# Kernel tuning notes

Hardware: AMD Instinct MI355X
Metric: run time of the kernel (lower is better)

Reference implementation:

```python
import jax, jax.numpy as jnp
import numpy as np

B, T_ENC, C, H, NSTEPS, NCLS, NEMB = 512, 64, 512, 512, 26, 97, 256


def setup_inputs() -> dict:
    key = jax.random.key(0)
    ks = jax.random.split(key, 20)
    w = lambda k, shape, s=0.05: jax.random.normal(k, shape, dtype=jnp.float32) * s
    return {
        "batch_H": jax.random.normal(ks[0], (B, T_ENC, C), dtype=jnp.float32),
        "Attentive_Sequence": jax.random.normal(ks[1], (B, NSTEPS, H), dtype=jnp.float32),
        "text": jax.random.randint(ks[2], (B, NSTEPS), 0, NCLS),
        "W_i2h": w(ks[3], (H, C)),                      # i2h, bias=False
        "W_h2h": w(ks[4], (H, H)), "b_h2h": w(ks[5], (H,)),
        "w_score": w(ks[6], (H,)),                      # score Linear(H,1), bias=False
        "W_ih": w(ks[7], (4 * H, C + NEMB)), "W_hh": w(ks[8], (4 * H, H)),
        "b_ih": w(ks[9], (4 * H,)), "b_hh": w(ks[10], (4 * H,)),
        "Wf1": w(ks[11], (H, H)), "bf1": w(ks[12], (H,)),   # GatedBimodal branch 1
        "Wf2": w(ks[13], (H, H)), "bf2": w(ks[14], (H,)),   # GatedBimodal branch 2
        "Wz": w(ks[15], (H, 2 * H)), "bz": w(ks[16], (H,)),  # gate over concat
        "W_gen": w(ks[17], (NCLS, H)), "b_gen": w(ks[18], (NCLS,)),
        "emb_table": w(ks[19], (NCLS + 1, NEMB), 1.0),
    }


def reference(batch_H, Attentive_Sequence, text, W_i2h, W_h2h, b_h2h, w_score,
              W_ih, W_hh, b_ih, b_hh, Wf1, bf1, Wf2, bf2, Wz, bz,
              W_gen, b_gen, emb_table):
    b = batch_H.shape[0]
    char_embs = emb_table[text]                                  # [B, NSTEPS, NEMB]
    H_proj = jnp.einsum('btc,hc->bth', batch_H, W_i2h)           # i2h once (loop-invariant)
    h0 = jnp.zeros((b, H), jnp.float32)
    c0 = jnp.zeros((b, H), jnp.float32)

    def step(carry, xs):
        h, c = carry
        emb_t, seq_t = xs                                        # [B,NEMB], [B,H]
        hp = h @ W_h2h.T + b_h2h                                 # h2h
        e = jnp.tanh(H_proj + hp[:, None, :]) @ w_score          # [B, T_ENC]
        alpha = jax.nn.softmax(e, axis=1)
        context = jnp.einsum('bt,btc->bc', alpha, batch_H)       # bmm(alpha^T, H)
        # GatedBimodal fusion
        f1 = jnp.tanh(context @ Wf1.T + bf1)
        f2 = jnp.tanh(seq_t @ Wf2.T + bf2)
        z = jax.nn.sigmoid(jnp.concatenate([context, seq_t], axis=1) @ Wz.T + bz)
        I_char = z * f1 + (1.0 - z) * f2
        # LSTMCell
        x = jnp.concatenate([I_char, emb_t], axis=1)
        gates = x @ W_ih.T + b_ih + h @ W_hh.T + b_hh
        i_g, f_g, g_g, o_g = jnp.split(gates, 4, axis=1)
        c_new = jax.nn.sigmoid(f_g) * c + jax.nn.sigmoid(i_g) * jnp.tanh(g_g)
        h_new = jax.nn.sigmoid(o_g) * jnp.tanh(c_new)
        return (h_new, c_new), (h_new, alpha, I_char)

    xs = (jnp.swapaxes(char_embs, 0, 1), jnp.swapaxes(Attentive_Sequence, 0, 1))
    _, (hs, alphas, chars) = jax.lax.scan(step, (h0, c0), xs)
    output_hiddens = jnp.swapaxes(hs, 0, 1)                      # [B, NSTEPS, H]
    seq_attention_map = jnp.transpose(alphas, (1, 2, 0))         # [B, T_ENC, NSTEPS]
    Char = jnp.swapaxes(chars, 0, 1)                             # [B, NSTEPS, H]
    probs = output_hiddens @ W_gen.T + b_gen                     # [B, NSTEPS, NCLS]
    return probs, seq_attention_map, output_hiddens, Char
```

## Files before the change

### kernel.cpp

```cpp
#include <hip/hip_runtime.h>

#define NS_ 26
#define NCLS_ 97

typedef short bf16x8 __attribute__((ext_vector_type(8)));
typedef float f32x4 __attribute__((ext_vector_type(4)));

__device__ __forceinline__ unsigned short f2bf(float f) {
  union { float f; unsigned u; } v; v.f = f;
  unsigned r = v.u + 0x7fffu + ((v.u >> 16) & 1u);
  return (unsigned short)(r >> 16);
}
__device__ __forceinline__ float bf2f(unsigned short h) {
  union { unsigned u; float f; } v; v.u = ((unsigned)h) << 16;
  return v.f;
}
__device__ __forceinline__ float sigm_f(float x) { return 1.f / (1.f + __expf(-x)); }
__device__ __forceinline__ float tanh_f(float x) { return 1.f - 2.f / (1.f + __expf(2.f * x)); }

__device__ __forceinline__ void gl_lds16(const void* g, void* l) {
  __builtin_amdgcn_global_load_lds(
      (const __attribute__((address_space(1))) unsigned int*)g,
      (__attribute__((address_space(3))) unsigned int*)l, 16, 0, 0);
}

template <bool OUTF>
__global__ __launch_bounds__(256) void gemm_tiled_k(
    const unsigned short* __restrict__ Ag, const unsigned short* __restrict__ Bg,
    const float* __restrict__ bias, float* __restrict__ outF,
    unsigned short* __restrict__ outB, int K, long ldo, int Nvalid) {
  __shared__ unsigned short As[128 * 64];
  __shared__ unsigned short Bs[128 * 64];
  const int tid = threadIdx.x;
  const int w = tid >> 6, l = tid & 63;
  const int l15 = l & 15, lq = l >> 4;
  const int wm = w >> 1, wn = w & 1;
  const long rowBase = (long)blockIdx.y * 128;
  const long colBase = (long)blockIdx.x * 128;
  const int lrow = l >> 3, ps_st = l & 7;
  f32x4 acc[4][4] = {};
  for (int kt = 0; kt < K; kt += 64) {
#pragma unroll
    for (int i = 0; i < 4; ++i) {
      const int row = i * 32 + w * 8 + lrow;
      const int ls = ps_st ^ (row & 7);
      gl_lds16(Ag + (rowBase + row) * K + kt + ls * 8, As + i * 2048 + w * 512);
      gl_lds16(Bg + (colBase + row) * K + kt + ls * 8, Bs + i * 2048 + w * 512);
    }
    __syncthreads();
#pragma unroll
    for (int kh = 0; kh < 2; ++kh) {
      bf16x8 af[4], bfr[4];
#pragma unroll
      for (int mi = 0; mi < 4; ++mi) {
        const int row = wm * 64 + mi * 16 + l15;
        const int ps = (kh * 4 + lq) ^ (row & 7);
        af[mi] = *(const bf16x8*)(As + row * 64 + ps * 8);
      }
#pragma unroll
      for (int ni = 0; ni < 4; ++ni) {
        const int row = wn * 64 + ni * 16 + l15;
        const int ps = (kh * 4 + lq) ^ (row & 7);
        bfr[ni] = *(const bf16x8*)(Bs + row * 64 + ps * 8);
      }
#pragma unroll
      for (int mi = 0; mi < 4; ++mi)
#pragma unroll
        for (int ni = 0; ni < 4; ++ni)
          acc[mi][ni] = __builtin_amdgcn_mfma_f32_16x16x32_bf16(af[mi], bfr[ni], acc[mi][ni], 0, 0, 0);
    }
    __syncthreads();
  }
#pragma unroll
  for (int mi = 0; mi < 4; ++mi)
#pragma unroll
    for (int ni = 0; ni < 4; ++ni) {
      const long gcol = colBase + wn * 64 + ni * 16 + l15;
      if (gcol >= Nvalid) continue;
      const float bv = bias ? bias[gcol] : 0.f;
#pragma unroll
      for (int r = 0; r < 4; ++r) {
        const long grow = rowBase + wm * 64 + mi * 16 + lq * 4 + r;
        const float v = acc[mi][ni][r] + bv;
        if (OUTF) outF[grow * ldo + gcol] = v;
        else      outB[grow * ldo + gcol] = f2bf(v);
      }
    }
}

__global__ __launch_bounds__(1024, 4) void attn_fused_k(
    const unsigned short* __restrict__ hrd, const unsigned short* __restrict__ Wt4,
    const float* __restrict__ b_h2h, const unsigned short* __restrict__ Hproj,
    const unsigned short* __restrict__ bH, const float* __restrict__ w_score,
    float* __restrict__ attn_map, unsigned short* __restrict__ ctx, int s) {
  const long b0 = (long)blockIdx.x * 2;
  const int tid = threadIdx.x;
  __shared__ float hs[1024];
  __shared__ float hp_t[1040];
  __shared__ float ws_t[520];
  __shared__ float e_s[128];
  __shared__ float csum[1024];
  hs[tid] = bf2f(hrd[b0 * 512 + tid]);
  if (tid < 512) ws_t[(tid & 7) * 65 + (tid >> 3)] = w_score[tid];
  __syncthreads();
  {
    const int pair = tid >> 9, j = tid & 511;
    float acc = b_h2h[j];
    const unsigned short* wp = Wt4 + j * 4;
    const float* hv0 = hs + pair * 512;
#pragma unroll 8
    for (int k4 = 0; k4 < 128; ++k4) {
      const ushort4 wv = *(const ushort4*)(wp + k4 * 2048);
      const f32x4 hv = *(const f32x4*)(hv0 + k4 * 4);
      acc += bf2f(wv.x) * hv[0] + bf2f(wv.y) * hv[1]
           + bf2f(wv.z) * hv[2] + bf2f(wv.w) * hv[3];
    }
    hp_t[pair * 520 + (j & 7) * 65 + (j >> 3)] = acc;
  }
  __syncthreads();
  const int w16 = tid >> 6, l = tid & 63;
  const int srow = w16 >> 3;
  const float* hpT = hp_t + srow * 520;
#pragma unroll
  for (int tt = 0; tt < 8; ++tt) {
    const int t = (w16 & 7) * 8 + tt;
    const bf16x8 hv = *(const bf16x8*)(Hproj + ((b0 + srow) * 64 + t) * 512 + l * 8);
    float acc = 0.f;
#pragma unroll
    for (int j = 0; j < 8; ++j)
      acc += tanh_f(bf2f((unsigned short)hv[j]) + hpT[j * 65 + l]) * ws_t[j * 65 + l];
    acc += __shfl_xor(acc, 1);
    acc += __shfl_xor(acc, 2);
    acc += __shfl_xor(acc, 4);
    acc += __shfl_xor(acc, 8);
    acc += __shfl_xor(acc, 16);
    acc += __shfl_xor(acc, 32);
    if (l == 0) e_s[srow * 64 + t] = acc;
  }
  __syncthreads();
  if ((w16 & 7) == 0) {
    const int row = w16 >> 3;
    const float e = e_s[row * 64 + l];
    float m = e;
    for (int off = 32; off; off >>= 1) m = fmaxf(m, __shfl_xor(m, off));
    const float p = __expf(e - m);
    float sum = p;
    for (int off = 32; off; off >>= 1) sum += __shfl_xor(sum, off);
    const float a = p / sum;
    e_s[row * 64 + l] = a;
    attn_map[((b0 + row) * 64 + l) * NS_ + s] = a;
  }
  __syncthreads();
  {
    const int row = tid >> 9, st = tid & 511;
    const int half = st >> 8, jj = st & 255;
    float c0 = 0.f, c1 = 0.f;
    const unsigned* bhp = (const unsigned*)(bH + ((b0 + row) * 64 + half * 32) * 512) + jj;
    const float* al = e_s + row * 64 + half * 32;
#pragma unroll 8
    for (int t = 0; t < 32; ++t) {
      const float a = al[t];
      const unsigned pv = bhp[(long)t * 256];
      c0 += a * bf2f((unsigned short)(pv & 0xffffu));
      c1 += a * bf2f((unsigned short)(pv >> 16));
    }
    if (half) { csum[row * 512 + jj * 2] = c0; csum[row * 512 + jj * 2 + 1] = c1; }
    __syncthreads();
    if (!half) {
      c0 += csum[row * 512 + jj * 2];
      c1 += csum[row * 512 + jj * 2 + 1];
      ((unsigned*)ctx)[(b0 + row) * 256 + jj] = (unsigned)f2bf(c0) | ((unsigned)f2bf(c1) << 16);
    }
  }
}

__global__ __launch_bounds__(512, 4) void gated_fused_k(
    const unsigned short* __restrict__ ctx, const unsigned short* __restrict__ Wfz,
    const unsigned short* __restrict__ FZpre, const float* __restrict__ bf1,
    unsigned short* __restrict__ Ichar, float* __restrict__ Char_out, int s) {
  __shared__ float ls[2 * 16 * 65];
  const int tid = threadIdx.x, w = tid >> 6, l = tid & 63, l15 = l & 15, lq = l >> 4;
  const int b0 = blockIdx.y * 16, j0 = blockIdx.x * 64;
  const int which = w >> 2, nh = w & 3;
  f32x4 acc = {};
  const long arow = b0 + l15;
  const long gw = (long)(which ? 512 : 0) + j0 + nh * 16 + l15;
#pragma unroll
  for (int kt = 0; kt < 512; kt += 64) {
    const int k0 = kt + lq * 8, k1 = k0 + 32;
    const bf16x8 a0 = *(const bf16x8*)(ctx + arow * 512 + k0);
    const bf16x8 a1 = *(const bf16x8*)(ctx + arow * 512 + k1);
    const bf16x8 w0 = *(const bf16x8*)(Wfz + gw * 512 + k0);
    const bf16x8 w1 = *(const bf16x8*)(Wfz + gw * 512 + k1);
    acc = __builtin_amdgcn_mfma_f32_16x16x32_bf16(a0, w0, acc, 0, 0, 0);
    acc = __builtin_amdgcn_mfma_f32_16x16x32_bf16(a1, w1, acc, 0, 0, 0);
  }
#pragma unroll
  for (int r = 0; r < 4; ++r)
    ls[which * 1040 + (lq * 4 + r) * 65 + nh * 16 + l15] = acc[r];
  __syncthreads();
#pragma unroll
  for (int i = 0; i < 2; ++i) {
    const int e = tid + i * 512;
    const int r = e >> 6, c = e & 63;
    const long b = b0 + r;
    const int j = j0 + c;
    const float f1 = tanh_f(ls[r * 65 + c] + bf1[j]);
    const float zc = ls[1040 + r * 65 + c];
    const long pr = (b * NS_ + s) * 1024;
    const float f2 = tanh_f(bf2f(FZpre[pr + j]));
    const float z = sigm_f(zc + bf2f(FZpre[pr + 512 + j]));
    const float I = z * f1 + (1.f - z) * f2;
    Char_out[(b * NS_ + s) * 512 + j] = I;
    Ichar[b * 512 + j] = f2bf(I);
  }
}

__global__ __launch_bounds__(512, 4) void gates_lstm_k(
    const unsigned short* __restrict__ Ichar, const unsigned short* __restrict__ embb,
    const unsigned short* __restrict__ hrd, const unsigned short* __restrict__ Wihh,
    const float* __restrict__ biasG, float* __restrict__ cbuf,
    float* __restrict__ hid_out, unsigned short* __restrict__ hwr, int s) {
  __shared__ float gs[4 * 32 * 33];
  const int tid = threadIdx.x, w = tid >> 6, l = tid & 63, l15 = l & 15, lq = l >> 4;
  const int b0 = blockIdx.y * 32, j0 = blockIdx.x * 32;
  const int g = w & 3, mi = w >> 2;
  const long arow = b0 + mi * 16 + l15;
  const unsigned short* iptr = Ichar + arow * 512;
  const unsigned short* eptr = embb + (arow * NS_ + s) * 256 - 512;
  const unsigned short* hptr = hrd + arow * 512 - 768;
  const unsigned short* wptr = Wihh + ((long)g * 512 + j0 + l15) * 1280;
  f32x4 acc[2] = {};
#pragma unroll
  for (int kt = 0; kt < 1280; kt += 64) {
    const int k0 = kt + lq * 8, k1 = k0 + 32;
    bf16x8 a0, a1, b0r[2], b1r[2];
    a0 = (k0 < 512) ? *(const bf16x8*)(iptr + k0)
       : (k0 < 768) ? *(const bf16x8*)(eptr + k0)
                    : *(const bf16x8*)(hptr + k0);
    a1 = (k1 < 512) ? *(const bf16x8*)(iptr + k1)
       : (k1 < 768) ? *(const bf16x8*)(eptr + k1)
                    : *(const bf16x8*)(hptr + k1);
#pragma unroll
    for (int ni = 0; ni < 2; ++ni) {
      b0r[ni] = *(const bf16x8*)(wptr + (long)ni * 16 * 1280 + k0);
      b1r[ni] = *(const bf16x8*)(wptr + (long)ni * 16 * 1280 + k1);
    }
#pragma unroll
    for (int ni = 0; ni < 2; ++ni) {
      acc[ni] = __builtin_amdgcn_mfma_f32_16x16x32_bf16(a0, b0r[ni], acc[ni], 0, 0, 0);
      acc[ni] = __builtin_amdgcn_mfma_f32_16x16x32_bf16(a1, b1r[ni], acc[ni], 0, 0, 0);
    }
  }
#pragma unroll
  for (int ni = 0; ni < 2; ++ni)
#pragma unroll
    for (int r = 0; r < 4; ++r) {
      const int rl = mi * 16 + lq * 4 + r;
      const int cl = ni * 16 + l15;
      gs[(g * 32 + rl) * 33 + cl] = acc[ni][r];
    }
  __syncthreads();
#pragma unroll
  for (int i = 0; i < 2; ++i) {
    const int e = tid + i * 512;
    const int r = e >> 5, c = e & 31;
    const long b = b0 + r;
    const int j = j0 + c;
    const float ig = sigm_f(gs[(0 * 32 + r) * 33 + c] + biasG[j]);
    const float fg = sigm_f(gs[(1 * 32 + r) * 33 + c] + biasG[512 + j]);
    const float gg = tanh_f(gs[(2 * 32 + r) * 33 + c] + biasG[1024 + j]);
    const float og = sigm_f(gs[(3 * 32 + r) * 33 + c] + biasG[1536 + j]);
    const float cn = fg * cbuf[b * 512 + j] + ig * gg;
    cbuf[b * 512 + j] = cn;
    const float h = og * tanh_f(cn);
    hid_out[(b * NS_ + s) * 512 + j] = h;
    hwr[b * 512 + j] = f2bf(h);
  }
}

__global__ __launch_bounds__(256) void probs_k(
    const float* __restrict__ Af, const unsigned short* __restrict__ Wg,
    const float* __restrict__ bias, float* __restrict__ outp) {
  const int tid = threadIdx.x, w = tid >> 6, l = tid & 63, l15 = l & 15, lq = l >> 4;
  const long mrow = (long)blockIdx.y * 64 + w * 16 + l15;
  const int nbase = blockIdx.x * 64;
  f32x4 acc[4] = {};
  for (int kt = 0; kt < 512; kt += 32) {
    const int k = kt + lq * 8;
    const float4 av0 = *(const float4*)(Af + mrow * 512 + k);
    const float4 av1 = *(const float4*)(Af + mrow * 512 + k + 4);
    bf16x8 a;
    a[0] = (short)f2bf(av0.x); a[1] = (short)f2bf(av0.y);
    a[2] = (short)f2bf(av0.z); a[3] = (short)f2bf(av0.w);
    a[4] = (short)f2bf(av1.x); a[5] = (short)f2bf(av1.y);
    a[6] = (short)f2bf(av1.z); a[7] = (short)f2bf(av1.w);
#pragma unroll
    for (int nb = 0; nb < 4; ++nb) {
      const bf16x8 b = *(const bf16x8*)(Wg + (long)(nbase + nb * 16 + l15) * 512 + k);
      acc[nb] = __builtin_amdgcn_mfma_f32_16x16x32_bf16(a, b, acc[nb], 0, 0, 0);
    }
  }
#pragma unroll
  for (int nb = 0; nb < 4; ++nb) {
    const int colg = nbase + nb * 16 + l15;
    if (colg >= NCLS_) continue;
    const float bv = bias[colg];
#pragma unroll
    for (int r = 0; r < 4; ++r) {
      const long rowg = (long)blockIdx.y * 64 + w * 16 + lq * 4 + r;
      outp[rowg * NCLS_ + colg] = acc[nb][r] + bv;
    }
  }
}

#define CVT_N0 4194304L
#define CVT_N1 1703936L
#define CVT_N2 65536L
__global__ void mega_cvt_k(const float* __restrict__ batch_H, const float* __restrict__ AS,
                           const float* __restrict__ W_i2h,
                           unsigned short* __restrict__ bH, unsigned short* __restrict__ ASb,
                           unsigned short* __restrict__ Wi2hb) {
  const long q = (long)blockIdx.x * 256 + threadIdx.x;
  const float* src; unsigned short* dst; long i;
  if (q < CVT_N0) { src = batch_H; dst = bH; i = q; }
  else if (q < CVT_N0 + CVT_N1) { src = AS; dst = ASb; i = q - CVT_N0; }
  else if (q < CVT_N0 + CVT_N1 + CVT_N2) { src = W_i2h; dst = Wi2hb; i = q - CVT_N0 - CVT_N1; }
  else return;
  const float4 v = *(const float4*)(src + i * 4);
  ushort4 o;
  o.x = f2bf(v.x); o.y = f2bf(v.y); o.z = f2bf(v.z); o.w = f2bf(v.w);
  *(ushort4*)(dst + i * 4) = o;
}

#define PK_N0 2621440L
#define PK_N1 524288L
#define PK_N2 524288L
#define PK_N3 65536L
#define PK_N4 262144L
#define PK_N5 3072L
#define PK_N6 3407872L
__global__ void mega_pack_k(
    const float* __restrict__ W_ih, const float* __restrict__ W_hh,
    const float* __restrict__ Wf1, const float* __restrict__ Wf2,
    const float* __restrict__ Wz, const float* __restrict__ W_gen,
    const float* __restrict__ W_h2h,
    const float* __restrict__ b_ih, const float* __restrict__ b_hh,
    const float* __restrict__ bf2, const float* __restrict__ bz,
    const float* __restrict__ emb_table, const int* __restrict__ text,
    unsigned short* __restrict__ Wihh, unsigned short* __restrict__ Wfz,
    unsigned short* __restrict__ Wfz2, unsigned short* __restrict__ Wgenb,
    unsigned short* __restrict__ Wt4, float* __restrict__ biasG,
    float* __restrict__ biasFZ, unsigned short* __restrict__ embb) {
  long q = (long)blockIdx.x * 256 + threadIdx.x;
  if (q < PK_N0) {
    const int row = (int)(q / 1280), c = (int)(q % 1280);
    const float v = (c < 768) ? W_ih[(long)row * 768 + c] : W_hh[(long)row * 512 + (c - 768)];
    Wihh[q] = f2bf(v);
    return;
  }
  q -= PK_N0;
  if (q < PK_N1) {
    const int row = (int)(q >> 9), k = (int)(q & 511);
    const float v = (row < 512) ? Wf1[(long)row * 512 + k] : Wz[(long)(row - 512) * 1024 + k];
    Wfz[q] = f2bf(v);
    return;
  }
  q -= PK_N1;
  if (q < PK_N2) {
    const int row = (int)(q >> 9), k = (int)(q & 511);
    const float v = (row < 512) ? Wf2[(long)row * 512 + k]
                                : Wz[(long)(row - 512) * 1024 + 512 + k];
    Wfz2[q] = f2bf(v);
    return;
  }
  q -= PK_N2;
  if (q < PK_N3) {
    const int row = (int)(q >> 9), k = (int)(q & 511);
    Wgenb[q] = (row < NCLS_) ? f2bf(W_gen[(long)row * 512 + k]) : (unsigned short)0;
    return;
  }
  q -= PK_N3;
  if (q < PK_N4) {
    const int j = (int)(q >> 9), k = (int)(q & 511);
    Wt4[((long)(k >> 2) * 2048) + j * 4 + (k & 3)] = f2bf(W_h2h[q]);
    return;
  }
  q -= PK_N4;
  if (q < PK_N5) {
    if (q < 2048) biasG[q] = b_ih[q] + b_hh[q];
    else {
      const int j = (int)(q - 2048);
      biasFZ[j] = (j < 512) ? bf2[j] : bz[j - 512];
    }
    return;
  }
  q -= PK_N5;
  if (q < PK_N6) {
    const long bs = q >> 8;
    const int j = (int)(q & 255);
    const int t = text[bs];
    embb[q] = f2bf(emb_table[(long)t * 256 + j]);
  }
}

extern "C" void kernel_launch(void* const* d_in, const int* in_sizes, int n_in,
                              void* d_out, int out_size, void* d_ws, size_t ws_size,
                              hipStream_t stream) {
  (void)in_sizes; (void)n_in; (void)out_size; (void)ws_size;
  const float* batch_H  = (const float*)d_in[0];
  const float* AS       = (const float*)d_in[1];
  const int*   text     = (const int*)d_in[2];
  const float* W_i2h    = (const float*)d_in[3];
  const float* W_h2h    = (const float*)d_in[4];
  const float* b_h2h    = (const float*)d_in[5];
  const float* w_score  = (const float*)d_in[6];
  const float* W_ih     = (const float*)d_in[7];
  const float* W_hh     = (const float*)d_in[8];
  const float* b_ih     = (const float*)d_in[9];
  const float* b_hh     = (const float*)d_in[10];
  const float* Wf1      = (const float*)d_in[11];
  const float* bf1      = (const float*)d_in[12];
  const float* Wf2      = (const float*)d_in[13];
  const float* bf2      = (const float*)d_in[14];
  const float* Wz       = (const float*)d_in[15];
  const float* bz       = (const float*)d_in[16];
  const float* W_gen    = (const float*)d_in[17];
  const float* b_gen    = (const float*)d_in[18];
  const float* emb_tab  = (const float*)d_in[19];

  float* out = (float*)d_out;
  float* out_probs = out;
  float* out_attn  = out + 1291264;
  float* out_hid   = out + 2143232;
  float* out_char  = out + 8958976;

  char* wsp = (char*)d_ws;
  auto alloc = [&](size_t bytes) { char* p = wsp; wsp += (bytes + 255) & ~(size_t)255; return p; };
  unsigned short* bH    = (unsigned short*)alloc(33554432);
  unsigned short* Hproj = (unsigned short*)alloc(33554432);
  unsigned short* ASb   = (unsigned short*)alloc(13631488);
  unsigned short* embb  = (unsigned short*)alloc(6815744);
  unsigned short* FZpre = (unsigned short*)alloc(27262976);
  unsigned short* Wt4   = (unsigned short*)alloc(524288);
  unsigned short* Wfz   = (unsigned short*)alloc(1048576);
  unsigned short* Wfz2  = (unsigned short*)alloc(1048576);
  unsigned short* Wihh  = (unsigned short*)alloc(5242880);
  unsigned short* Wgenb = (unsigned short*)alloc(131072);
  unsigned short* Wi2hb = (unsigned short*)alloc(524288);
  float* biasG          = (float*)alloc(8192);
  float* biasFZ         = (float*)alloc(4096);
  char* ab = (char*)ASb;
  unsigned short* ctx   = (unsigned short*)(ab);
  unsigned short* Ichar = (unsigned short*)(ab + 524288);
  float* cbuf           = (float*)(ab + 1048576);
  unsigned short* hbuf  = (unsigned short*)(ab + 2097152);

  mega_cvt_k<<<dim3(23297), dim3(256), 0, stream>>>(batch_H, AS, W_i2h, bH, ASb, Wi2hb);
  mega_pack_k<<<dim3(28960), dim3(256), 0, stream>>>(
      W_ih, W_hh, Wf1, Wf2, Wz, W_gen, W_h2h, b_ih, b_hh, bf2, bz, emb_tab, text,
      Wihh, Wfz, Wfz2, Wgenb, Wt4, biasG, biasFZ, embb);

  gemm_tiled_k<false><<<dim3(4, 256), dim3(256), 0, stream>>>(
      bH, Wi2hb, nullptr, nullptr, Hproj, 512, 512, 512);

  gemm_tiled_k<false><<<dim3(8, 104), dim3(256), 0, stream>>>(
      ASb, Wfz2, biasFZ, nullptr, FZpre, 512, 1024, 1024);

  hipMemsetAsync(cbuf, 0, 1048576, stream);
  hipMemsetAsync(hbuf, 0, 1048576, stream);

  for (int s = 0; s < NS_; ++s) {
    unsigned short* hrd = hbuf + (s & 1) * 262144;
    unsigned short* hwr = hbuf + ((s + 1) & 1) * 262144;
    attn_fused_k<<<dim3(256), dim3(1024), 0, stream>>>(
        hrd, Wt4, b_h2h, Hproj, bH, w_score, out_attn, ctx, s);
    gated_fused_k<<<dim3(8, 32), dim3(512), 0, stream>>>(
        ctx, Wfz, FZpre, bf1, Ichar, out_char, s);
    gates_lstm_k<<<dim3(16, 16), dim3(512), 0, stream>>>(
        Ichar, embb, hrd, Wihh, biasG, cbuf, out_hid, hwr, s);
  }

  probs_k<<<dim3(2, 208), dim3(256), 0, stream>>>(out_hid, Wgenb, b_gen, out_probs);
}
```

Before: 2.010 ms.

## Fuse per-step recurrent kernels into one persistent cooperative kernel with group barriers

Replaces the 78 per-step kernel launches (attention, gated fusion, LSTM gates) with a single cooperative kernel that loops over all 26 steps. The batch is split into 8 independent groups of 32 blocks, each synchronised by a hand-written atomic barrier, and shared intermediates go through global memory with cache-bypassing loads and stores. The h2h projection becomes a separate MFMA phase that writes hp to global memory. This removes launch overhead and inter-kernel gaps, but adds four grid barriers per step, relies on all blocks being co-resident, and runs 1024-thread blocks with some threads idle in several phases.

```diff
diff --git a/kernel.cpp b/kernel.cpp
--- a/kernel.cpp
+++ b/kernel.cpp
@@ -22,6 +22,39 @@
   __builtin_amdgcn_global_load_lds(
       (const __attribute__((address_space(1))) unsigned int*)g,
       (__attribute__((address_space(3))) unsigned int*)l, 16, 0, 0);
+}
+
+__device__ __forceinline__ bf16x8 llcld(const unsigned short* p) {
+  bf16x8 v;
+  asm volatile("global_load_dwordx4 %0, %1, off sc0 sc1\ns_waitcnt vmcnt(0)"
+               : "=v"(v) : "v"(p) : "memory");
+  return v;
+}
+__device__ __forceinline__ void llcst(unsigned short* p, bf16x8 v) {
+  asm volatile("global_store_dwordx4 %0, %1, off sc0 sc1" :: "v"(p), "v"(v) : "memory");
+}
+__device__ __forceinline__ f32x4 llcldf(const float* p) {
+  f32x4 v;
+  asm volatile("global_load_dwordx4 %0, %1, off sc0 sc1\ns_waitcnt vmcnt(0)"
+               : "=v"(v) : "v"(p) : "memory");
+  return v;
+}
+__device__ __forceinline__ void llcstf(float* p, f32x4 v) {
+  asm volatile("global_store_dwordx4 %0, %1, off sc0 sc1" :: "v"(p), "v"(v) : "memory");
+}
+
+__device__ __forceinline__ void gbar(unsigned* bar, unsigned* gen, unsigned target) {
+  asm volatile("s_waitcnt vmcnt(0)" ::: "memory");
+  __syncthreads();
+  if (threadIdx.x == 0) {
+    const unsigned prev = __hip_atomic_fetch_add(bar, 1u, __ATOMIC_RELAXED, __HIP_MEMORY_SCOPE_AGENT);
+    if (prev + 1u == target * 32u) {
+      __hip_atomic_store(gen, target, __ATOMIC_RELAXED, __HIP_MEMORY_SCOPE_AGENT);
+    } else {
+      while (__hip_atomic_load(gen, __ATOMIC_RELAXED, __HIP_MEMORY_SCOPE_AGENT) < target) {}
+    }
+  }
+  __syncthreads();
 }
 
 template <bool OUTF>
@@ -88,194 +121,302 @@
     }
 }
 
-__global__ __launch_bounds__(1024, 4) void attn_fused_k(
-    const unsigned short* __restrict__ hrd, const unsigned short* __restrict__ Wt4,
-    const float* __restrict__ b_h2h, const unsigned short* __restrict__ Hproj,
-    const unsigned short* __restrict__ bH, const float* __restrict__ w_score,
-    float* __restrict__ attn_map, unsigned short* __restrict__ ctx, int s) {
-  const long b0 = (long)blockIdx.x * 2;
+struct CoopArgs {
+  const unsigned short* Hproj;
+  const unsigned short* bH;
+  const unsigned short* Wh2hb;
+  const unsigned short* Wfz;
+  const unsigned short* FZpre;
+  const unsigned short* Wihh;
+  const unsigned short* embb;
+  const float* b_h2h;
+  const float* w_score;
+  const float* bf1;
+  const float* biasG;
+  float* hp;
+  float* out_attn;
+  float* out_char;
+  float* out_hid;
+  float* cbuf;
+  unsigned short* ctx;
+  unsigned short* Ichar;
+  unsigned short* hbuf;
+  unsigned* bars;
+};
+
+__global__ __launch_bounds__(1024, 4) void scan_coop_k(CoopArgs A) {
+  __shared__ float ws_t[520];
+  __shared__ __align__(16) char smraw[52224];
   const int tid = threadIdx.x;
-  __shared__ float hs[1024];
-  __shared__ float hp_t[1040];
-  __shared__ float ws_t[520];
-  __shared__ float e_s[128];
-  __shared__ float csum[1024];
-  hs[tid] = bf2f(hrd[b0 * 512 + tid]);
-  if (tid < 512) ws_t[(tid & 7) * 65 + (tid >> 3)] = w_score[tid];
+  const int bx = blockIdx.x;
+  const int g = bx & 7, lb = bx >> 3;
+  const long rb = (long)g * 64;
+  unsigned* bar = A.bars + g * 32;
+  unsigned* gen = bar + 1;
+  unsigned tgt = 0;
+
+  if (tid < 512) ws_t[(tid & 7) * 65 + (tid >> 3)] = A.w_score[tid];
   __syncthreads();
-  {
-    const int pair = tid >> 9, j = tid & 511;
-    float acc = b_h2h[j];
-    const unsigned short* wp = Wt4 + j * 4;
-    const float* hv0 = hs + pair * 512;
+
+  for (int s = 0; s < NS_; ++s) {
+    const unsigned short* hrd = A.hbuf + (s & 1) * 262144;
+    unsigned short* hwr = A.hbuf + ((s + 1) & 1) * 262144;
+
+    {
+      const int bt = lb >> 3, jt = lb & 7;
+      const long b0 = rb + bt * 16;
+      const int j0 = jt * 64;
+      unsigned short* h16 = (unsigned short*)smraw;
+      float* ls = (float*)(smraw + 16640);
+      float* hpo = (float*)(smraw + 24960);
+      {
+        const int row = tid >> 6, c = tid & 63;
+        const bf16x8 v = llcld(hrd + (b0 + row) * 512 + c * 8);
+        *(bf16x8*)(h16 + row * 520 + c * 8) = v;
+      }
+      __syncthreads();
+      if (tid < 512) {
+        const int w = tid >> 6, l = tid & 63, l15 = l & 15, lq = l >> 4;
+        const int kh = w >> 2, ni = w & 3;
+        const unsigned short* wrow = A.Wh2hb + (long)(j0 + ni * 16 + l15) * 512 + kh * 256;
+        const unsigned short* arow = h16 + l15 * 520 + kh * 256;
+        f32x4 acc = {};
+#pragma unroll
+        for (int kt = 0; kt < 256; kt += 64) {
+          const int k0 = kt + lq * 8, k1 = k0 + 32;
+          const bf16x8 a0 = *(const bf16x8*)(arow + k0);
+          const bf16x8 a1 = *(const bf16x8*)(arow + k1);
+          const bf16x8 w0 = *(const bf16x8*)(wrow + k0);
+          const bf16x8 w1 = *(const bf16x8*)(wrow + k1);
+          acc = __builtin_amdgcn_mfma_f32_16x16x32_bf16(a0, w0, acc, 0, 0, 0);
+          acc = __builtin_amdgcn_mfma_f32_16x16x32_bf16(a1, w1, acc, 0, 0, 0);
+        }
+#pragma unroll
+        for (int r = 0; r < 4; ++r)
+          ls[kh * 1040 + (lq * 4 + r) * 65 + ni * 16 + l15] = acc[r];
+      }
+      __syncthreads();
+      {
+        const int r = tid >> 6, c = tid & 63;
+        hpo[r * 64 + c] = ls[r * 65 + c] + ls[1040 + r * 65 + c] + A.b_h2h[j0 + c];
+      }
+      __syncthreads();
+      if (tid < 256) {
+        const int row = tid >> 4, c = tid & 15;
+        const f32x4 v = *(const f32x4*)(hpo + row * 64 + c * 4);
+        llcstf(A.hp + (b0 + row) * 512 + j0 + c * 4, v);
+      }
+    }
+    gbar(bar, gen, ++tgt);
+
+    {
+      const long b0 = rb + lb * 2;
+      float* hp_t = (float*)smraw;
+      float* e_s  = (float*)(smraw + 4160);
+      float* csum = (float*)(smraw + 4672);
+      unsigned* pck = (unsigned*)(smraw + 8768);
+      if (tid < 256) {
+        const int row = tid >> 7, q = tid & 127;
+        const f32x4 v = llcldf(A.hp + (b0 + row) * 512 + q * 4);
+#pragma unroll
+        for (int i = 0; i < 4; ++i) {
+          const int j = q * 4 + i;
+          hp_t[row * 520 + (j & 7) * 65 + (j >> 3)] = v[i];
+        }
+      }
+      __syncthreads();
+      const int w16 = tid >> 6, l = tid & 63;
+      const int srow = w16 >> 3;
+      const float* hpT = hp_t + srow * 520;
+#pragma unroll
+      for (int tt = 0; tt < 8; ++tt) {
+        const int t = (w16 & 7) * 8 + tt;
+        const bf16x8 hv = *(const bf16x8*)(A.Hproj + ((b0 + srow) * 64 + t) * 512 + l * 8);
+        float acc = 0.f;
+#pragma unroll
+        for (int j = 0; j < 8; ++j)
+          acc += tanh_f(bf2f((unsigned short)hv[j]) + hpT[j * 65 + l]) * ws_t[j * 65 + l];
+        acc += __shfl_xor(acc, 1);
+        acc += __shfl_xor(acc, 2);
+        acc += __shfl_xor(acc, 4);
+        acc += __shfl_xor(acc, 8);
+        acc += __shfl_xor(acc, 16);
+        acc += __shfl_xor(acc, 32);
+        if (l == 0) e_s[srow * 64 + t] = acc;
+      }
+      __syncthreads();
+      if ((w16 & 7) == 0) {
+        const float e = e_s[srow * 64 + l];
+        float m = e;
+        for (int off = 32; off; off >>= 1) m = fmaxf(m, __shfl_xor(m, off));
+        const float p = __expf(e - m);
+        float sum = p;
+        for (int off = 32; off; off >>= 1) sum += __shfl_xor(sum, off);
+        const float a = p / sum;
+        e_s[srow * 64 + l] = a;
+        A.out_attn[((b0 + srow) * 64 + l) * NS_ + s] = a;
+      }
+      __syncthreads();
+      {
+        const int row = tid >> 9, st = tid & 511;
+        const int half = st >> 8, jj = st & 255;
+        float c0 = 0.f, c1 = 0.f;
+        const unsigned* bhp = (const unsigned*)(A.bH + ((b0 + row) * 64 + half * 32) * 512) + jj;
+        const float* al = e_s + row * 64 + half * 32;
 #pragma unroll 8
-    for (int k4 = 0; k4 < 128; ++k4) {
-      const ushort4 wv = *(const ushort4*)(wp + k4 * 2048);
-      const f32x4 hv = *(const f32x4*)(hv0 + k4 * 4);
-      acc += bf2f(wv.x) * hv[0] + bf2f(wv.y) * hv[1]
-           + bf2f(wv.z) * hv[2] + bf2f(wv.w) * hv[3];
-    }
-    hp_t[pair * 520 + (j & 7) * 65 + (j >> 3)] = acc;
-  }
-  __syncthreads();
-  const int w16 = tid >> 6, l = tid & 63;
-  const int srow = w16 >> 3;
-  const float* hpT = hp_t + srow * 520;
-#pragma unroll
-  for (int tt = 0; tt < 8; ++tt) {
-    const int t = (w16 & 7) * 8 + tt;
-    const bf16x8 hv = *(const bf16x8*)(Hproj + ((b0 + srow) * 64 + t) * 512 + l * 8);
-    float acc = 0.f;
-#pragma unroll
-    for (int j = 0; j < 8; ++j)
-      acc += tanh_f(bf2f((unsigned short)hv[j]) + hpT[j * 65 + l]) * ws_t[j * 65 + l];
-    acc += __shfl_xor(acc, 1);
-    acc += __shfl_xor(acc, 2);
-    acc += __shfl_xor(acc, 4);
-    acc += __shfl_xor(acc, 8);
-    acc += __shfl_xor(acc, 16);
-    acc += __shfl_xor(acc, 32);
-    if (l == 0) e_s[srow * 64 + t] = acc;
-  }
-  __syncthreads();
-  if ((w16 & 7) == 0) {
-    const int row = w16 >> 3;
-    const float e = e_s[row * 64 + l];
-    float m = e;
-    for (int off = 32; off; off >>= 1) m = fmaxf(m, __shfl_xor(m, off));
-    const float p = __expf(e - m);
-    float sum = p;
-    for (int off = 32; off; off >>= 1) sum += __shfl_xor(sum, off);
-    const float a = p / sum;
-    e_s[row * 64 + l] = a;
-    attn_map[((b0 + row) * 64 + l) * NS_ + s] = a;
-  }
-  __syncthreads();
-  {
-    const int row = tid >> 9, st = tid & 511;
-    const int half = st >> 8, jj = st & 255;
-    float c0 = 0.f, c1 = 0.f;
-    const unsigned* bhp = (const unsigned*)(bH + ((b0 + row) * 64 + half * 32) * 512) + jj;
-    const float* al = e_s + row * 64 + half * 32;
-#pragma unroll 8
-    for (int t = 0; t < 32; ++t) {
-      const float a = al[t];
-      const unsigned pv = bhp[(long)t * 256];
-      c0 += a * bf2f((unsigned short)(pv & 0xffffu));
-      c1 += a * bf2f((unsigned short)(pv >> 16));
-    }
-    if (half) { csum[row * 512 + jj * 2] = c0; csum[row * 512 + jj * 2 + 1] = c1; }
-    __syncthreads();
-    if (!half) {
-      c0 += csum[row * 512 + jj * 2];
-      c1 += csum[row * 512 + jj * 2 + 1];
-      ((unsigned*)ctx)[(b0 + row) * 256 + jj] = (unsigned)f2bf(c0) | ((unsigned)f2bf(c1) << 16);
-    }
-  }
-}
-
-__global__ __launch_bounds__(512, 4) void gated_fused_k(
-    const unsigned short* __restrict__ ctx, const unsigned short* __restrict__ Wfz,
-    const unsigned short* __restrict__ FZpre, const float* __restrict__ bf1,
-    unsigned short* __restrict__ Ichar, float* __restrict__ Char_out, int s) {
-  __shared__ float ls[2 * 16 * 65];
-  const int tid = threadIdx.x, w = tid >> 6, l = tid & 63, l15 = l & 15, lq = l >> 4;
-  const int b0 = blockIdx.y * 16, j0 = blockIdx.x * 64;
-  const int which = w >> 2, nh = w & 3;
-  f32x4 acc = {};
-  const long arow = b0 + l15;
-  const long gw = (long)(which ? 512 : 0) + j0 + nh * 16 + l15;
-#pragma unroll
-  for (int kt = 0; kt < 512; kt += 64) {
-    const int k0 = kt + lq * 8, k1 = k0 + 32;
-    const bf16x8 a0 = *(const bf16x8*)(ctx + arow * 512 + k0);
-    const bf16x8 a1 = *(const bf16x8*)(ctx + arow * 512 + k1);
-    const bf16x8 w0 = *(const bf16x8*)(Wfz + gw * 512 + k0);
-    const bf16x8 w1 = *(const bf16x8*)(Wfz + gw * 512 + k1);
-    acc = __builtin_amdgcn_mfma_f32_16x16x32_bf16(a0, w0, acc, 0, 0, 0);
-    acc = __builtin_amdgcn_mfma_f32_16x16x32_bf16(a1, w1, acc, 0, 0, 0);
-  }
-#pragma unroll
-  for (int r = 0; r < 4; ++r)
-    ls[which * 1040 + (lq * 4 + r) * 65 + nh * 16 + l15] = acc[r];
-  __syncthreads();
-#pragma unroll
-  for (int i = 0; i < 2; ++i) {
-    const int e = tid + i * 512;
-    const int r = e >> 6, c = e & 63;
-    const long b = b0 + r;
-    const int j = j0 + c;
-    const float f1 = tanh_f(ls[r * 65 + c] + bf1[j]);
-    const float zc = ls[1040 + r * 65 + c];
-    const long pr = (b * NS_ + s) * 1024;
-    const float f2 = tanh_f(bf2f(FZpre[pr + j]));
-    const float z = sigm_f(zc + bf2f(FZpre[pr + 512 + j]));
-    const float I = z * f1 + (1.f - z) * f2;
-    Char_out[(b * NS_ + s) * 512 + j] = I;
-    Ichar[b * 512 + j] = f2bf(I);
-  }
-}
-
-__global__ __launch_bounds__(512, 4) void gates_lstm_k(
-    const unsigned short* __restrict__ Ichar, const unsigned short* __restrict__ embb,
-    const unsigned short* __restrict__ hrd, const unsigned short* __restrict__ Wihh,
-    const float* __restrict__ biasG, float* __restrict__ cbuf,
-    float* __restrict__ hid_out, unsigned short* __restrict__ hwr, int s) {
-  __shared__ float gs[4 * 32 * 33];
-  const int tid = threadIdx.x, w = tid >> 6, l = tid & 63, l15 = l & 15, lq = l >> 4;
-  const int b0 = blockIdx.y * 32, j0 = blockIdx.x * 32;
-  const int g = w & 3, mi = w >> 2;
-  const long arow = b0 + mi * 16 + l15;
-  const unsigned short* iptr = Ichar + arow * 512;
-  const unsigned short* eptr = embb + (arow * NS_ + s) * 256 - 512;
-  const unsigned short* hptr = hrd + arow * 512 - 768;
-  const unsigned short* wptr = Wihh + ((long)g * 512 + j0 + l15) * 1280;
-  f32x4 acc[2] = {};
-#pragma unroll
-  for (int kt = 0; kt < 1280; kt += 64) {
-    const int k0 = kt + lq * 8, k1 = k0 + 32;
-    bf16x8 a0, a1, b0r[2], b1r[2];
-    a0 = (k0 < 512) ? *(const bf16x8*)(iptr + k0)
-       : (k0 < 768) ? *(const bf16x8*)(eptr + k0)
-                    : *(const bf16x8*)(hptr + k0);
-    a1 = (k1 < 512) ? *(const bf16x8*)(iptr + k1)
-       : (k1 < 768) ? *(const bf16x8*)(eptr + k1)
-                    : *(const bf16x8*)(hptr + k1);
-#pragma unroll
-    for (int ni = 0; ni < 2; ++ni) {
-      b0r[ni] = *(const bf16x8*)(wptr + (long)ni * 16 * 1280 + k0);
-      b1r[ni] = *(const bf16x8*)(wptr + (long)ni * 16 * 1280 + k1);
-    }
-#pragma unroll
-    for (int ni = 0; ni < 2; ++ni) {
-      acc[ni] = __builtin_amdgcn_mfma_f32_16x16x32_bf16(a0, b0r[ni], acc[ni], 0, 0, 0);
-      acc[ni] = __builtin_amdgcn_mfma_f32_16x16x32_bf16(a1, b1r[ni], acc[ni], 0, 0, 0);
-    }
-  }
-#pragma unroll
-  for (int ni = 0; ni < 2; ++ni)
-#pragma unroll
-    for (int r = 0; r < 4; ++r) {
-      const int rl = mi * 16 + lq * 4 + r;
-      const int cl = ni * 16 + l15;
-      gs[(g * 32 + rl) * 33 + cl] = acc[ni][r];
-    }
-  __syncthreads();
-#pragma unroll
-  for (int i = 0; i < 2; ++i) {
-    const int e = tid + i * 512;
-    const int r = e >> 5, c = e & 31;
-    const long b = b0 + r;
-    const int j = j0 + c;
-    const float ig = sigm_f(gs[(0 * 32 + r) * 33 + c] + biasG[j]);
-    const float fg = sigm_f(gs[(1 * 32 + r) * 33 + c] + biasG[512 + j]);
-    const float gg = tanh_f(gs[(2 * 32 + r) * 33 + c] + biasG[1024 + j]);
-    const float og = sigm_f(gs[(3 * 32 + r) * 33 + c] + biasG[1536 + j]);
-    const float cn = fg * cbuf[b * 512 + j] + ig * gg;
-    cbuf[b * 512 + j] = cn;
-    const float h = og * tanh_f(cn);
-    hid_out[(b * NS_ + s) * 512 + j] = h;
-    hwr[b * 512 + j] = f2bf(h);
+        for (int t = 0; t < 32; ++t) {
+          const float a = al[t];
+          const unsigned pv = bhp[(long)t * 256];
+          c0 += a * bf2f((unsigned short)(pv & 0xffffu));
+          c1 += a * bf2f((unsigned short)(pv >> 16));
+        }
+        if (half) { csum[row * 512 + jj * 2] = c0; csum[row * 512 + jj * 2 + 1] = c1; }
+        __syncthreads();
+        if (!half) {
+          c0 += csum[row * 512 + jj * 2];
+          c1 += csum[row * 512 + jj * 2 + 1];
+          pck[row * 256 + jj] = (unsigned)f2bf(c0) | ((unsigned)f2bf(c1) << 16);
+        }
+      }
+      __syncthreads();
+      if (tid < 128) {
+        const int row = tid >> 6, c = tid & 63;
+        bf16x8 v;
+        const unsigned* src = pck + row * 256 + c * 4;
+        ((unsigned*)&v)[0] = src[0]; ((unsigned*)&v)[1] = src[1];
+        ((unsigned*)&v)[2] = src[2]; ((unsigned*)&v)[3] = src[3];
+        llcst(A.ctx + (b0 + row) * 512 + c * 8, v);
+      }
+    }
+    gbar(bar, gen, ++tgt);
+
+    {
+      const int j0 = (lb & 7) * 64;
+      const long b0 = rb + (lb >> 3) * 16;
+      unsigned short* ctxs = (unsigned short*)smraw;
+      float* ls = (float*)(smraw + 16640);
+      unsigned short* ist = (unsigned short*)(smraw + 24960);
+      {
+        const int row = tid >> 6, c = tid & 63;
+        const bf16x8 v = llcld(A.ctx + (b0 + row) * 512 + c * 8);
+        *(bf16x8*)(ctxs + row * 520 + c * 8) = v;
+      }
+      __syncthreads();
+      if (tid < 512) {
+        const int w = tid >> 6, l = tid & 63, l15 = l & 15, lq = l >> 4;
+        const int which = w >> 2, nh = w & 3;
+        f32x4 acc = {};
+        const long gw = (long)(which ? 512 : 0) + j0 + nh * 16 + l15;
+#pragma unroll
+        for (int kt = 0; kt < 512; kt += 64) {
+          const int k0 = kt + lq * 8, k1 = k0 + 32;
+          const bf16x8 a0 = *(const bf16x8*)(ctxs + l15 * 520 + k0);
+          const bf16x8 a1 = *(const bf16x8*)(ctxs + l15 * 520 + k1);
+          const bf16x8 w0 = *(const bf16x8*)(A.Wfz + gw * 512 + k0);
+          const bf16x8 w1 = *(const bf16x8*)(A.Wfz + gw * 512 + k1);
+          acc = __builtin_amdgcn_mfma_f32_16x16x32_bf16(a0, w0, acc, 0, 0, 0);
+          acc = __builtin_amdgcn_mfma_f32_16x16x32_bf16(a1, w1, acc, 0, 0, 0);
+        }
+#pragma unroll
+        for (int r = 0; r < 4; ++r)
+          ls[which * 1040 + (lq * 4 + r) * 65 + nh * 16 + l15] = acc[r];
+      }
+      __syncthreads();
+      {
+        const int r = tid >> 6, c = tid & 63;
+        const long b = b0 + r;
+        const int j = j0 + c;
+        const float f1 = tanh_f(ls[r * 65 + c] + A.bf1[j]);
+        const float zc = ls[1040 + r * 65 + c];
+        const long pr = (b * NS_ + s) * 1024;
+        const float f2 = tanh_f(bf2f(A.FZpre[pr + j]));
+        const float z = sigm_f(zc + bf2f(A.FZpre[pr + 512 + j]));
+        const float I = z * f1 + (1.f - z) * f2;
+        A.out_char[(b * NS_ + s) * 512 + j] = I;
+        ist[r * 64 + c] = f2bf(I);
+      }
+      __syncthreads();
+      if (tid < 128) {
+        const int row = tid >> 3, c = tid & 7;
+        const bf16x8 v = *(const bf16x8*)(ist + row * 64 + c * 8);
+        llcst(A.Ichar + (b0 + row) * 512 + j0 + c * 8, v);
+      }
+    }
+    gbar(bar, gen, ++tgt);
+
+    {
+      const int bt = lb & 3, jp = lb >> 2;
+      const long b0 = rb + bt * 16;
+      unsigned short* ichs = (unsigned short*)smraw;
+      unsigned short* hss = (unsigned short*)(smraw + 16640);
+      float* gs = (float*)(smraw + 33280);
+      unsigned short* hst = (unsigned short*)(smraw + 50176);
+      for (int t = tid; t < 2048; t += 1024) {
+        const int arr = t >> 10, q = t & 1023;
+        const int row = q >> 6, c = q & 63;
+        if (arr == 0) {
+          const bf16x8 v = llcld(A.Ichar + (b0 + row) * 512 + c * 8);
+          *(bf16x8*)(ichs + row * 520 + c * 8) = v;
+        } else {
+          const bf16x8 v = llcld(hrd + (b0 + row) * 512 + c * 8);
+          *(bf16x8*)(hss + row * 520 + c * 8) = v;
+        }
+      }
+      __syncthreads();
+      {
+        const int sb = tid >> 9, st = tid & 511;
+        const int w = st >> 6, l = st & 63, l15 = l & 15, lq = l >> 4;
+        const int g4 = w & 3, ni = w >> 2;
+        const int j0 = jp * 64 + sb * 32;
+        const unsigned short* wptr = A.Wihh + ((long)g4 * 512 + j0 + ni * 16 + l15) * 1280;
+        const unsigned short* eptr = A.embb + ((b0 + l15) * NS_ + s) * 256;
+        f32x4 acc = {};
+#pragma unroll
+        for (int kt = 0; kt < 1280; kt += 64) {
+          const int k0 = kt + lq * 8, k1 = k0 + 32;
+          bf16x8 a0, a1;
+          a0 = (k0 < 512) ? *(const bf16x8*)(ichs + l15 * 520 + k0)
+             : (k0 < 768) ? *(const bf16x8*)(eptr + (k0 - 512))
+                          : *(const bf16x8*)(hss + l15 * 520 + (k0 - 768));
+          a1 = (k1 < 512) ? *(const bf16x8*)(ichs + l15 * 520 + k1)
+             : (k1 < 768) ? *(const bf16x8*)(eptr + (k1 - 512))
+                          : *(const bf16x8*)(hss + l15 * 520 + (k1 - 768));
+          const bf16x8 w0 = *(const bf16x8*)(wptr + k0);
+          const bf16x8 w1 = *(const bf16x8*)(wptr + k1);
+          acc = __builtin_amdgcn_mfma_f32_16x16x32_bf16(a0, w0, acc, 0, 0, 0);
+          acc = __builtin_amdgcn_mfma_f32_16x16x32_bf16(a1, w1, acc, 0, 0, 0);
+        }
+        float* gss = gs + sb * 2112;
+#pragma unroll
+        for (int r = 0; r < 4; ++r)
+          gss[(g4 * 16 + lq * 4 + r) * 33 + ni * 16 + l15] = acc[r];
+      }
+      __syncthreads();
+      {
+        const int sb = tid >> 9, e = tid & 511;
+        const int r = e >> 5, c = e & 31;
+        const long b = b0 + r;
+        const int j = jp * 64 + sb * 32 + c;
+        const float* gss = gs + sb * 2112;
+        const float ig = sigm_f(gss[(0 * 16 + r) * 33 + c] + A.biasG[j]);
+        const float fg = sigm_f(gss[(1 * 16 + r) * 33 + c] + A.biasG[512 + j]);
+        const float gg = tanh_f(gss[(2 * 16 + r) * 33 + c] + A.biasG[1024 + j]);
+        const float og = sigm_f(gss[(3 * 16 + r) * 33 + c] + A.biasG[1536 + j]);
+        const float cn = fg * A.cbuf[b * 512 + j] + ig * gg;
+        A.cbuf[b * 512 + j] = cn;
+        const float h = og * tanh_f(cn);
+        A.out_hid[(b * NS_ + s) * 512 + j] = h;
+        hst[sb * 512 + r * 32 + c] = f2bf(h);
+      }
+      __syncthreads();
+      if (tid < 128) {
+        const int sb = tid >> 6, q = tid & 63;
+        const int row = q >> 2, c = q & 3;
+        const bf16x8 v = *(const bf16x8*)(hst + sb * 512 + row * 32 + c * 8);
+        llcst(hwr + (b0 + row) * 512 + jp * 64 + sb * 32 + c * 8, v);
+      }
+    }
+    gbar(bar, gen, ++tgt);
   }
 }
 
@@ -350,7 +491,7 @@
     const float* __restrict__ emb_table, const int* __restrict__ text,
     unsigned short* __restrict__ Wihh, unsigned short* __restrict__ Wfz,
     unsigned short* __restrict__ Wfz2, unsigned short* __restrict__ Wgenb,
-    unsigned short* __restrict__ Wt4, float* __restrict__ biasG,
+    unsigned short* __restrict__ Wh2hb, float* __restrict__ biasG,
     float* __restrict__ biasFZ, unsigned short* __restrict__ embb) {
   long q = (long)blockIdx.x * 256 + threadIdx.x;
   if (q < PK_N0) {
@@ -382,8 +523,7 @@
   }
   q -= PK_N3;
   if (q < PK_N4) {
-    const int j = (int)(q >> 9), k = (int)(q & 511);
-    Wt4[((long)(k >> 2) * 2048) + j * 4 + (k & 3)] = f2bf(W_h2h[q]);
+    Wh2hb[q] = f2bf(W_h2h[q]);
     return;
   }
   q -= PK_N4;
@@ -442,7 +582,7 @@
   unsigned short* ASb   = (unsigned short*)alloc(13631488);
   unsigned short* embb  = (unsigned short*)alloc(6815744);
   unsigned short* FZpre = (unsigned short*)alloc(27262976);
-  unsigned short* Wt4   = (unsigned short*)alloc(524288);
+  unsigned short* Wh2hb = (unsigned short*)alloc(524288);
   unsigned short* Wfz   = (unsigned short*)alloc(1048576);
   unsigned short* Wfz2  = (unsigned short*)alloc(1048576);
   unsigned short* Wihh  = (unsigned short*)alloc(5242880);
@@ -450,16 +590,18 @@
   unsigned short* Wi2hb = (unsigned short*)alloc(524288);
   float* biasG          = (float*)alloc(8192);
   float* biasFZ         = (float*)alloc(4096);
+  unsigned* bars        = (unsigned*)alloc(1024);
   char* ab = (char*)ASb;
   unsigned short* ctx   = (unsigned short*)(ab);
   unsigned short* Ichar = (unsigned short*)(ab + 524288);
   float* cbuf           = (float*)(ab + 1048576);
   unsigned short* hbuf  = (unsigned short*)(ab + 2097152);
+  float* hp             = (float*)(ab + 3145728);
 
   mega_cvt_k<<<dim3(23297), dim3(256), 0, stream>>>(batch_H, AS, W_i2h, bH, ASb, Wi2hb);
   mega_pack_k<<<dim3(28960), dim3(256), 0, stream>>>(
       W_ih, W_hh, Wf1, Wf2, Wz, W_gen, W_h2h, b_ih, b_hh, bf2, bz, emb_tab, text,
-      Wihh, Wfz, Wfz2, Wgenb, Wt4, biasG, biasFZ, embb);
+      Wihh, Wfz, Wfz2, Wgenb, Wh2hb, biasG, biasFZ, embb);
 
   gemm_tiled_k<false><<<dim3(4, 256), dim3(256), 0, stream>>>(
       bH, Wi2hb, nullptr, nullptr, Hproj, 512, 512, 512);
@@ -469,17 +611,16 @@
 
   hipMemsetAsync(cbuf, 0, 1048576, stream);
   hipMemsetAsync(hbuf, 0, 1048576, stream);
-
-  for (int s = 0; s < NS_; ++s) {
-    unsigned short* hrd = hbuf + (s & 1) * 262144;
-    unsigned short* hwr = hbuf + ((s + 1) & 1) * 262144;
-    attn_fused_k<<<dim3(256), dim3(1024), 0, stream>>>(
-        hrd, Wt4, b_h2h, Hproj, bH, w_score, out_attn, ctx, s);
-    gated_fused_k<<<dim3(8, 32), dim3(512), 0, stream>>>(
-        ctx, Wfz, FZpre, bf1, Ichar, out_char, s);
-    gates_lstm_k<<<dim3(16, 16), dim3(512), 0, stream>>>(
-        Ichar, embb, hrd, Wihh, biasG, cbuf, out_hid, hwr, s);
-  }
+  hipMemsetAsync(bars, 0, 1024, stream);
+
+  CoopArgs ca;
+  ca.Hproj = Hproj; ca.bH = bH; ca.Wh2hb = Wh2hb; ca.Wfz = Wfz; ca.FZpre = FZpre;
+  ca.Wihh = Wihh; ca.embb = embb;
+  ca.b_h2h = b_h2h; ca.w_score = w_score; ca.bf1 = bf1; ca.biasG = biasG;
+  ca.hp = hp; ca.out_attn = out_attn; ca.out_char = out_char; ca.out_hid = out_hid;
+  ca.cbuf = cbuf; ca.ctx = ctx; ca.Ichar = Ichar; ca.hbuf = hbuf; ca.bars = bars;
+  void* kargs[] = { (void*)&ca };
+  hipLaunchCooperativeKernel((const void*)scan_coop_k, dim3(256), dim3(1024), kargs, 0, stream);
 
   probs_k<<<dim3(2, 208), dim3(256), 0, stream>>>(out_hid, Wgenb, b_gen, out_probs);
 }
```

After: 1.665 ms. 1.21x faster.
